# Performance work log

Hardware: AMD Instinct MI355X
Metric: run time of the kernel (lower is better)

Reference implementation:

```python
import jax, jax.numpy as jnp
import numpy as np

B, S, H, NH, F = 4, 1024, 1024, 16, 4096
HD = H // NH
PAD = 128  # last PAD positions are padding


def layer_norm(x, g, b, eps=1e-5):
    mu = jnp.mean(x, axis=-1, keepdims=True)
    var = jnp.mean(jnp.square(x - mu), axis=-1, keepdims=True)
    return (x - mu) * jax.lax.rsqrt(var + eps) * g + b


def setup_inputs() -> dict:
    key = jax.random.key(0)
    ks = jax.random.split(key, 10)
    sc = 0.02
    x = jax.random.normal(ks[0], (B, S, H), dtype=jnp.float32)
    attn_bias = jax.random.normal(ks[1], (B, S, S), dtype=jnp.float32)
    key_padding_mask = jnp.broadcast_to(jnp.arange(S) >= (S - PAD), (B, S))
    return {
        "x": x,
        "attn_bias": attn_bias,
        "key_padding_mask": key_padding_mask,
        "qkv_w": jax.random.normal(ks[2], (H, 3 * H), dtype=jnp.float32) * sc,
        "qkv_b": jnp.zeros((3 * H,), jnp.float32),
        "proj_w": jax.random.normal(ks[3], (H, H), dtype=jnp.float32) * sc,
        "proj_b": jnp.zeros((H,), jnp.float32),
        "ln1_g": jnp.ones((H,), jnp.float32),
        "ln1_b": jnp.zeros((H,), jnp.float32),
        "ln2_g": jnp.ones((H,), jnp.float32),
        "ln2_b": jnp.zeros((H,), jnp.float32),
        "ffn_w1": jax.random.normal(ks[4], (H, F), dtype=jnp.float32) * sc,
        "ffn_b1": jnp.zeros((F,), jnp.float32),
        "ffn_w2": jax.random.normal(ks[5], (F, H), dtype=jnp.float32) * sc,
        "ffn_b2": jnp.zeros((H,), jnp.float32),
    }


def reference(x, attn_bias, key_padding_mask, qkv_w, qkv_b, proj_w, proj_b,
              ln1_g, ln1_b, ln2_g, ln2_b, ffn_w1, ffn_b1, ffn_w2, ffn_b2):
    scale = HD ** -0.5
    qkv = (x @ qkv_w + qkv_b).reshape(B, S, 3, NH, HD)
    q, k, v = (qkv[:, :, i].transpose(0, 2, 1, 3) for i in range(3))  # [B,NH,S,HD]
    scores = jnp.einsum('bhqd,bhkd->bhqk', q, k) * scale
    scores = scores + attn_bias[:, None, :, :]
    scores = jnp.where(key_padding_mask[:, None, None, :], -jnp.inf, scores)
    attn = jax.nn.softmax(scores, axis=-1)
    out = jnp.einsum('bhqk,bhkd->bhqd', attn, v)
    out = out.transpose(0, 2, 1, 3).reshape(B, S, H)
    out = out @ proj_w + proj_b
    x = layer_norm(x + out, ln1_g, ln1_b)
    h = jax.nn.gelu(x @ ffn_w1 + ffn_b1, approximate=False)
    x = layer_norm(x + (h @ ffn_w2 + ffn_b2), ln2_g, ln2_b)
    x = jnp.where(key_padding_mask[:, :, None], 0.0, x)
    return x
```

## Files before the change

kernel.cpp:

```cpp
#include <hip/hip_runtime.h>
#include <cstdint>
#include <cstddef>

#define SEQ    1024
#define HDIM   1024
#define NHEAD  16
#define HEADD  64
#define FDIM   4096
#define BROWS  4096
#define SACT   896

typedef unsigned short u16;
typedef __bf16 bf16x8 __attribute__((ext_vector_type(8)));
typedef float  f32x4  __attribute__((ext_vector_type(4)));

__device__ __forceinline__ float bf2f(u16 u) {
    union { float f; unsigned v; } x; x.v = ((unsigned)u) << 16; return x.f;
}
__device__ __forceinline__ u16 f2bf(float f) {
    union { float f; unsigned v; } x; x.f = f;
    unsigned r = x.v + 0x7FFFu + ((x.v >> 16) & 1u);
    return (u16)(r >> 16);
}

__device__ __forceinline__ f32x4 mfma16(bf16x8 a, bf16x8 b, f32x4 c) {
    return __builtin_amdgcn_mfma_f32_16x16x32_bf16(a, b, c, 0, 0, 0);
}

__device__ __forceinline__ void gload16(const void* g, void* lds) {
    __builtin_amdgcn_global_load_lds(
        (__attribute__((address_space(1))) void*)g,
        (__attribute__((address_space(3))) void*)lds,
        16, 0, 0);
}

__global__ void cvt_bf16_kernel(const float* __restrict__ in, u16* __restrict__ out) {
    int i = blockIdx.x * 256 + threadIdx.x;
    float4 v = ((const float4*)in)[i];
    ushort4 o;
    o.x = f2bf(v.x); o.y = f2bf(v.y); o.z = f2bf(v.z); o.w = f2bf(v.w);
    ((ushort4*)out)[i] = o;
}

__global__ void wcvt_kernel(const float* __restrict__ W, u16* __restrict__ WT, int K, int N) {
    __shared__ float t[32][33];
    int n0 = blockIdx.x * 32, k0 = blockIdx.y * 32;
    int tx = threadIdx.x, ty = threadIdx.y;
    #pragma unroll
    for (int i = 0; i < 32; i += 8)
        t[ty + i][tx] = W[(size_t)(k0 + ty + i) * N + n0 + tx];
    __syncthreads();
    #pragma unroll
    for (int i = 0; i < 32; i += 8)
        WT[(size_t)(n0 + ty + i) * K + k0 + tx] = f2bf(t[tx][ty + i]);
}

__global__ void transpose_v_kernel(const u16* __restrict__ qkv, u16* __restrict__ vt) {
    __shared__ u16 t[64][65];
    int bh = blockIdx.y, b = bh >> 4, h = bh & 15;
    int s0 = blockIdx.x << 6;
    int tid = threadIdx.x;
    #pragma unroll
    for (int it = 0; it < 16; ++it) {
        int idx = tid + (it << 8);
        int r = idx >> 6, c = idx & 63;
        t[r][c] = qkv[(size_t)(b * SEQ + s0 + r) * 3072 + 2048 + h * 64 + c];
    }
    __syncthreads();
    #pragma unroll
    for (int it = 0; it < 16; ++it) {
        int idx = tid + (it << 8);
        int hd = idx >> 6, s = idx & 63;
        vt[((size_t)bh * 64 + hd) * SEQ + s0 + s] = t[s][hd];
    }
}

template<int EPI, int SPLITK>
__global__ __launch_bounds__(256, 2)
void gemm_kernel(const u16* __restrict__ A, const u16* __restrict__ Bt,
                 const float* __restrict__ bias, const float* __restrict__ res,
                 void* __restrict__ out, float* __restrict__ out1,
                 int M, int N, int K)
{
    __shared__ char smem[32768];
    char* sA = smem;
    char* sB = smem + 16384;
    const int tid  = threadIdx.x;
    const int wv   = tid >> 6, ln = tid & 63;
    const int lcol = ln & 15, quad = ln >> 4;
    const int wy   = wv >> 1, wx = wv & 1;
    const int mbase = blockIdx.x << 7, nbase = blockIdx.y << 7;

    int kstart = 0, kend = K;
    if (SPLITK) { int kh = K >> 1; kstart = blockIdx.z * kh; kend = kstart + kh; }

    f32x4 acc[4][4];
    #pragma unroll
    for (int i = 0; i < 4; ++i)
        #pragma unroll
        for (int j = 0; j < 4; ++j)
            acc[i][j] = (f32x4){0.f, 0.f, 0.f, 0.f};

    for (int k0 = kstart; k0 < kend; k0 += 64) {
        __syncthreads();
        #pragma unroll
        for (int c = 0; c < 4; ++c) {
            int base = (c * 4 + wv) << 10;
            int flat = base + (ln << 4);
            int row  = flat >> 7;
            int g    = ((flat >> 4) & 7) ^ (row & 7);
            gload16(A  + (size_t)(mbase + row) * K + k0 + g * 8, sA + base);
            gload16(Bt + (size_t)(nbase + row) * K + k0 + g * 8, sB + base);
        }
        __syncthreads();
        #pragma unroll
        for (int ks = 0; ks < 2; ++ks) {
            bf16x8 af[4], bfr[4];
            #pragma unroll
            for (int t = 0; t < 4; ++t) {
                int row = (wy << 6) + (t << 4) + lcol;
                int ca  = ((ks << 2) + quad) ^ (row & 7);
                af[t] = *(const bf16x8*)(sA + row * 128 + ca * 16);
                int nrow = (wx << 6) + (t << 4) + lcol;
                int cb  = ((ks << 2) + quad) ^ (nrow & 7);
                bfr[t] = *(const bf16x8*)(sB + nrow * 128 + cb * 16);
            }
            #pragma unroll
            for (int i = 0; i < 4; ++i)
                #pragma unroll
                for (int j = 0; j < 4; ++j)
                    acc[i][j] = mfma16(af[i], bfr[j], acc[i][j]);
        }
    }

    const bool partial = SPLITK && (blockIdx.z == 1);
    #pragma unroll
    for (int i = 0; i < 4; ++i) {
        #pragma unroll
        for (int r = 0; r < 4; ++r) {
            int grow = mbase + (wy << 6) + (i << 4) + (quad << 2) + r;
            #pragma unroll
            for (int j = 0; j < 4; ++j) {
                int gcol = nbase + (wx << 6) + (j << 4) + lcol;
                float v = acc[i][j][r];
                if (partial) {
                    out1[(size_t)grow * N + gcol] = v;
                    continue;
                }
                v += bias[gcol];
                if (EPI == 1 || EPI == 3) v += res[(size_t)grow * N + gcol];
                if (EPI == 2) v = 0.5f * v * (1.0f + erff(v * 0.70710678f));
                if (EPI == 0 || EPI == 2)
                    ((u16*)out)[(size_t)grow * N + gcol] = f2bf(v);
                else
                    ((float*)out)[(size_t)grow * N + gcol] = v;
            }
        }
    }
}

__global__ __launch_bounds__(256, 4)
void attn_kernel(const u16* __restrict__ qkv, const u16* __restrict__ vt,
                 const float* __restrict__ bias, u16* __restrict__ out)
{
    __shared__ char sK[2][8192];
    __shared__ char sV[2][8192];
    __shared__ char pbuf[4][2048];
    const int tid  = threadIdx.x;
    const int wid  = tid >> 6, lane = tid & 63;
    const int lcol = lane & 15, quad = lane >> 4;
    const int bh = blockIdx.y, b = bh >> 4, h = bh & 15;
    const int q0 = (blockIdx.x << 6) + (wid << 4);
    char* pb = pbuf[wid];
    const float LOG2E = 1.44269504088896f;

    const u16* qrow = qkv + (size_t)(b * SEQ + q0 + lcol) * 3072 + h * 64;
    bf16x8 qf[2];
    #pragma unroll
    for (int half = 0; half < 2; ++half) {
        union { bf16x8 v; u16 u[8]; } a;
        a.v = *(const bf16x8*)(qrow + half * 32 + quad * 8);
        #pragma unroll
        for (int j = 0; j < 8; ++j) a.u[j] = f2bf(bf2f(a.u[j]) * (0.125f * LOG2E));
        qf[half] = a.v;
    }

    f32x4 o[4];
    #pragma unroll
    for (int nt = 0; nt < 4; ++nt) o[nt] = (f32x4){0.f, 0.f, 0.f, 0.f};
    float lsum[4] = {0.f, 0.f, 0.f, 0.f};

    const u16* khead = qkv + (size_t)b * SEQ * 3072 + 1024 + h * 64;
    const u16* vhead = vt + (size_t)bh * 64 * SEQ;
    const float* bbase = bias + ((size_t)b * SEQ + q0 + quad * 4) * SEQ + lcol;

    auto stage = [&](int kb, int bufi) {
        #pragma unroll
        for (int i = 0; i < 2; ++i) {
            int ck  = i * 256 + tid;
            int row = ck >> 3, c = ck & 7;
            int g   = c ^ (row & 7);
            gload16(khead + (size_t)(kb + row) * 3072 + g * 8, sK[bufi] + ck * 16);
            gload16(vhead + (size_t)row * SEQ + kb + g * 8,    sV[bufi] + ck * 16);
        }
    };

    stage(0, 0);
    float bpre[4][4];
    #pragma unroll
    for (int i = 0; i < 4; ++i)
        #pragma unroll
        for (int j = 0; j < 4; ++j)
            bpre[i][j] = bbase[(size_t)i * SEQ + 16 * j] * LOG2E;
    __syncthreads();

    const int NT = SACT / 64;
    for (int t = 0; t < NT; ++t) {
        const int cur = t & 1, nxt = cur ^ 1;
        const int kb  = t << 6;

        if (t + 1 < NT) stage(kb + 64, nxt);

        f32x4 sc[4];
        #pragma unroll
        for (int j = 0; j < 4; ++j) sc[j] = (f32x4){0.f, 0.f, 0.f, 0.f};
        #pragma unroll
        for (int ks = 0; ks < 2; ++ks)
            #pragma unroll
            for (int j = 0; j < 4; ++j) {
                int n = j * 16 + lcol;
                int c = ((ks << 2) + quad) ^ (n & 7);
                bf16x8 kf = *(const bf16x8*)(sK[cur] + n * 128 + c * 16);
                sc[j] = mfma16(qf[ks], kf, sc[j]);
            }

        #pragma unroll
        for (int j = 0; j < 4; ++j)
            #pragma unroll
            for (int i = 0; i < 4; ++i)
                sc[j][i] += bpre[i][j];

        if (t + 1 < NT) {
            #pragma unroll
            for (int i = 0; i < 4; ++i)
                #pragma unroll
                for (int j = 0; j < 4; ++j)
                    bpre[i][j] = bbase[(size_t)i * SEQ + kb + 64 + 16 * j] * LOG2E;
        }

        #pragma unroll
        for (int i = 0; i < 4; ++i) {
            int row = quad * 4 + i;
            #pragma unroll
            for (int j = 0; j < 4; ++j) {
                float p = __builtin_amdgcn_exp2f(sc[j][i]);
                lsum[i] += p;
                union { float f; unsigned v; } u; u.f = p;
                int col = lcol + 16 * j;
                int cch = (col >> 3) ^ (row & 7);
                *(u16*)(pb + row * 128 + cch * 16 + (col & 7) * 2)
                    = (u16)((u.v + 0x8000u) >> 16);
            }
        }

        #pragma unroll
        for (int ks = 0; ks < 2; ++ks) {
            int cp = ((ks << 2) + quad) ^ (lcol & 7);
            bf16x8 pa = *(const bf16x8*)(pb + lcol * 128 + cp * 16);
            #pragma unroll
            for (int nt = 0; nt < 4; ++nt) {
                int d = nt * 16 + lcol;
                int c = ((ks << 2) + quad) ^ (d & 7);
                bf16x8 vf = *(const bf16x8*)(sV[cur] + d * 128 + c * 16);
                o[nt] = mfma16(pa, vf, o[nt]);
            }
        }

        __syncthreads();
    }

    #pragma unroll
    for (int off = 1; off < 16; off <<= 1)
        #pragma unroll
        for (int i = 0; i < 4; ++i)
            lsum[i] += __shfl_xor(lsum[i], off);

    float inv[4];
    #pragma unroll
    for (int i = 0; i < 4; ++i) inv[i] = 1.0f / lsum[i];
    #pragma unroll
    for (int nt = 0; nt < 4; ++nt)
        #pragma unroll
        for (int i = 0; i < 4; ++i)
            out[(size_t)(b * SEQ + q0 + quad * 4 + i) * HDIM + h * 64 + nt * 16 + lcol]
                = f2bf(o[nt][i] * inv[i]);
}

template<int MODE, int ADD2>
__global__ void ln_kernel(const float* __restrict__ y, const float* __restrict__ y2,
                          const float* __restrict__ g, const float* __restrict__ bt,
                          float* __restrict__ of32, u16* __restrict__ obf)
{
    int row = blockIdx.x;
    int tid = threadIdx.x;
    if (MODE == 1) {
        int s = row & (SEQ - 1);
        if (s >= SACT) {
            float4 z = {0.f, 0.f, 0.f, 0.f};
            ((float4*)(of32 + (size_t)row * HDIM))[tid] = z;
            return;
        }
    }
    float4 v = ((const float4*)(y + (size_t)row * HDIM))[tid];
    if (ADD2) {
        float4 w = ((const float4*)(y2 + (size_t)row * HDIM))[tid];
        v.x += w.x; v.y += w.y; v.z += w.z; v.w += w.w;
    }
    float s1 = v.x + v.y + v.z + v.w;
    float s2 = v.x * v.x + v.y * v.y + v.z * v.z + v.w * v.w;
    #pragma unroll
    for (int off = 32; off >= 1; off >>= 1) {
        s1 += __shfl_xor(s1, off);
        s2 += __shfl_xor(s2, off);
    }
    __shared__ float rs[8];
    int wv = tid >> 6, ln = tid & 63;
    if (ln == 0) { rs[wv] = s1; rs[4 + wv] = s2; }
    __syncthreads();
    s1 = rs[0] + rs[1] + rs[2] + rs[3];
    s2 = rs[4] + rs[5] + rs[6] + rs[7];
    float mean = s1 * (1.0f / 1024.0f);
    float var  = s2 * (1.0f / 1024.0f) - mean * mean;
    float rstd = rsqrtf(var + 1e-5f);
    float4 gg = ((const float4*)g)[tid];
    float4 bb = ((const float4*)bt)[tid];
    float4 o;
    o.x = (v.x - mean) * rstd * gg.x + bb.x;
    o.y = (v.y - mean) * rstd * gg.y + bb.y;
    o.z = (v.z - mean) * rstd * gg.z + bb.z;
    o.w = (v.w - mean) * rstd * gg.w + bb.w;
    ((float4*)(of32 + (size_t)row * HDIM))[tid] = o;
    if (MODE == 0) {
        ushort4 ob;
        ob.x = f2bf(o.x); ob.y = f2bf(o.y); ob.z = f2bf(o.z); ob.w = f2bf(o.w);
        ((ushort4*)(obf + (size_t)row * HDIM))[tid] = ob;
    }
}

extern "C" void kernel_launch(void* const* d_in, const int* in_sizes, int n_in,
                              void* d_out, int out_size, void* d_ws, size_t ws_size,
                              hipStream_t stream)
{
    const float* x      = (const float*)d_in[0];
    const float* abias  = (const float*)d_in[1];
    const float* qkv_w  = (const float*)d_in[3];
    const float* qkv_b  = (const float*)d_in[4];
    const float* proj_w = (const float*)d_in[5];
    const float* proj_b = (const float*)d_in[6];
    const float* ln1_g  = (const float*)d_in[7];
    const float* ln1_b  = (const float*)d_in[8];
    const float* ln2_g  = (const float*)d_in[9];
    const float* ln2_b  = (const float*)d_in[10];
    const float* w1     = (const float*)d_in[11];
    const float* b1     = (const float*)d_in[12];
    const float* w2     = (const float*)d_in[13];
    const float* b2     = (const float*)d_in[14];
    float* out = (float*)d_out;

    char* ws = (char*)d_ws;
    const size_t MB = 1024 * 1024;
    u16*  xb     = (u16*)(ws + 0);
    u16*  aout   = xb;
    u16*  qkvb   = (u16*)(ws + 8 * MB);
    u16*  vtb    = (u16*)(ws + 32 * MB);
    u16*  hb     = (u16*)(ws + 8 * MB);
    u16*  wqkvT  = (u16*)(ws + 40 * MB);
    u16*  wprojT = (u16*)(ws + 46 * MB);
    u16*  w1T    = (u16*)(ws + 48 * MB);
    u16*  w2T    = (u16*)(ws + 56 * MB);
    u16*  x1b    = (u16*)(ws + 64 * MB);
    float* ybuf  = (float*)(ws + 72 * MB);
    float* x1f   = (float*)(ws + 88 * MB);
    float* pproj = (float*)(ws + 8 * MB);
    float* pffn2 = (float*)(ws + 40 * MB);
    (void)in_sizes; (void)n_in; (void)out_size; (void)ws_size;

    dim3 tb32(32, 8);
    cvt_bf16_kernel<<<4096, 256, 0, stream>>>(x, xb);
    wcvt_kernel<<<dim3(3072 / 32, 1024 / 32), tb32, 0, stream>>>(qkv_w, wqkvT, 1024, 3072);
    wcvt_kernel<<<dim3(1024 / 32, 1024 / 32), tb32, 0, stream>>>(proj_w, wprojT, 1024, 1024);
    wcvt_kernel<<<dim3(4096 / 32, 1024 / 32), tb32, 0, stream>>>(w1, w1T, 1024, 4096);
    wcvt_kernel<<<dim3(1024 / 32, 4096 / 32), tb32, 0, stream>>>(w2, w2T, 4096, 1024);
    gemm_kernel<0, 0><<<dim3(32, 24), 256, 0, stream>>>(xb, wqkvT, qkv_b, nullptr, qkvb, nullptr, BROWS, 3072, 1024);
    transpose_v_kernel<<<dim3(16, 64), 256, 0, stream>>>(qkvb, vtb);
    attn_kernel<<<dim3(16, 64), 256, 0, stream>>>(qkvb, vtb, abias, aout);
    gemm_kernel<1, 1><<<dim3(32, 8, 2), 256, 0, stream>>>(aout, wprojT, proj_b, x, ybuf, pproj, BROWS, 1024, 1024);
    ln_kernel<0, 1><<<4096, 256, 0, stream>>>(ybuf, pproj, ln1_g, ln1_b, x1f, x1b);
    gemm_kernel<2, 0><<<dim3(32, 32), 256, 0, stream>>>(x1b, w1T, b1, nullptr, hb, nullptr, BROWS, 4096, 1024);
    gemm_kernel<3, 1><<<dim3(32, 8, 2), 256, 0, stream>>>(hb, w2T, b2, x1f, ybuf, pffn2, BROWS, 1024, 4096);
    ln_kernel<1, 1><<<4096, 256, 0, stream>>>(ybuf, pffn2, ln2_g, ln2_b, out, nullptr);
}
```

Before: 366.4 us.

## Use 4-way split-K with bf16 partials reduced in fused layernorm, merge prep kernels

Raises split-K for the projection and FFN2 GEMMs from 2 to 4. Each split writes bf16 partials, and the layernorm kernel sums them together with the residual and bias. The five conversion and transpose launches are merged into one prep kernel. The aim is to fill more CUs on the N=1024 GEMMs and cut launch overhead. In exchange, partial sums are rounded to bf16, which loses some precision.

```diff
diff --git a/kernel.cpp b/kernel.cpp
--- a/kernel.cpp
+++ b/kernel.cpp
@@ -14,6 +14,8 @@
 typedef __bf16 bf16x8 __attribute__((ext_vector_type(8)));
 typedef float  f32x4  __attribute__((ext_vector_type(4)));
 
+struct P4 { u16* p0; u16* p1; u16* p2; u16* p3; };
+
 __device__ __forceinline__ float bf2f(u16 u) {
     union { float f; unsigned v; } x; x.v = ((unsigned)u) << 16; return x.f;
 }
@@ -34,18 +36,29 @@
         16, 0, 0);
 }
 
-__global__ void cvt_bf16_kernel(const float* __restrict__ in, u16* __restrict__ out) {
-    int i = blockIdx.x * 256 + threadIdx.x;
-    float4 v = ((const float4*)in)[i];
-    ushort4 o;
-    o.x = f2bf(v.x); o.y = f2bf(v.y); o.z = f2bf(v.z); o.w = f2bf(v.w);
-    ((ushort4*)out)[i] = o;
-}
-
-__global__ void wcvt_kernel(const float* __restrict__ W, u16* __restrict__ WT, int K, int N) {
+__global__ void prep_kernel(const float* __restrict__ x, u16* __restrict__ xb,
+                            const float* __restrict__ qkvw, u16* __restrict__ wqkvT,
+                            const float* __restrict__ projw, u16* __restrict__ wprojT,
+                            const float* __restrict__ w1, u16* __restrict__ w1T,
+                            const float* __restrict__ w2, u16* __restrict__ w2T)
+{
+    int bid = blockIdx.x, tid = threadIdx.x;
+    if (bid < 4096) {
+        int i = bid * 256 + tid;
+        float4 v = ((const float4*)x)[i];
+        ushort4 o;
+        o.x = f2bf(v.x); o.y = f2bf(v.y); o.z = f2bf(v.z); o.w = f2bf(v.w);
+        ((ushort4*)xb)[i] = o;
+        return;
+    }
+    const float* W; u16* WT; int K, N, bxx, byy;
+    if (bid < 7168)       { int l = bid - 4096;  W = qkvw;  WT = wqkvT;  K = 1024; N = 3072; bxx = l % 96;  byy = l / 96; }
+    else if (bid < 8192)  { int l = bid - 7168;  W = projw; WT = wprojT; K = 1024; N = 1024; bxx = l % 32;  byy = l / 32; }
+    else if (bid < 12288) { int l = bid - 8192;  W = w1;    WT = w1T;    K = 1024; N = 4096; bxx = l % 128; byy = l / 128; }
+    else                  { int l = bid - 12288; W = w2;    WT = w2T;    K = 4096; N = 1024; bxx = l % 32;  byy = l / 32; }
     __shared__ float t[32][33];
-    int n0 = blockIdx.x * 32, k0 = blockIdx.y * 32;
-    int tx = threadIdx.x, ty = threadIdx.y;
+    int tx = tid & 31, ty = tid >> 5;
+    int n0 = bxx * 32, k0 = byy * 32;
     #pragma unroll
     for (int i = 0; i < 32; i += 8)
         t[ty + i][tx] = W[(size_t)(k0 + ty + i) * N + n0 + tx];
@@ -78,9 +91,8 @@
 template<int EPI, int SPLITK>
 __global__ __launch_bounds__(256, 2)
 void gemm_kernel(const u16* __restrict__ A, const u16* __restrict__ Bt,
-                 const float* __restrict__ bias, const float* __restrict__ res,
-                 void* __restrict__ out, float* __restrict__ out1,
-                 int M, int N, int K)
+                 const float* __restrict__ bias, void* __restrict__ out,
+                 P4 parts, int M, int N, int K)
 {
     __shared__ char smem[32768];
     char* sA = smem;
@@ -92,7 +104,7 @@
     const int mbase = blockIdx.x << 7, nbase = blockIdx.y << 7;
 
     int kstart = 0, kend = K;
-    if (SPLITK) { int kh = K >> 1; kstart = blockIdx.z * kh; kend = kstart + kh; }
+    if (SPLITK > 1) { int kq = K / SPLITK; kstart = blockIdx.z * kq; kend = kstart + kq; }
 
     f32x4 acc[4][4];
     #pragma unroll
@@ -133,7 +145,10 @@
         }
     }
 
-    const bool partial = SPLITK && (blockIdx.z == 1);
+    u16* op = nullptr;
+    if (SPLITK > 1)
+        op = (blockIdx.z == 0) ? parts.p0 : (blockIdx.z == 1) ? parts.p1
+           : (blockIdx.z == 2) ? parts.p2 : parts.p3;
     #pragma unroll
     for (int i = 0; i < 4; ++i) {
         #pragma unroll
@@ -143,17 +158,13 @@
             for (int j = 0; j < 4; ++j) {
                 int gcol = nbase + (wx << 6) + (j << 4) + lcol;
                 float v = acc[i][j][r];
-                if (partial) {
-                    out1[(size_t)grow * N + gcol] = v;
-                    continue;
+                if (SPLITK > 1) {
+                    op[(size_t)grow * N + gcol] = f2bf(v);
+                } else {
+                    v += bias[gcol];
+                    if (EPI == 2) v = 0.5f * v * (1.0f + erff(v * 0.70710678f));
+                    ((u16*)out)[(size_t)grow * N + gcol] = f2bf(v);
                 }
-                v += bias[gcol];
-                if (EPI == 1 || EPI == 3) v += res[(size_t)grow * N + gcol];
-                if (EPI == 2) v = 0.5f * v * (1.0f + erff(v * 0.70710678f));
-                if (EPI == 0 || EPI == 2)
-                    ((u16*)out)[(size_t)grow * N + gcol] = f2bf(v);
-                else
-                    ((float*)out)[(size_t)grow * N + gcol] = v;
             }
         }
     }
@@ -296,10 +307,12 @@
                 = f2bf(o[nt][i] * inv[i]);
 }
 
-template<int MODE, int ADD2>
-__global__ void ln_kernel(const float* __restrict__ y, const float* __restrict__ y2,
-                          const float* __restrict__ g, const float* __restrict__ bt,
-                          float* __restrict__ of32, u16* __restrict__ obf)
+template<int MODE>
+__global__ void ln_fused_kernel(const u16* __restrict__ p0, const u16* __restrict__ p1,
+                                const u16* __restrict__ p2, const u16* __restrict__ p3,
+                                const float* __restrict__ res, const float* __restrict__ cb,
+                                const float* __restrict__ g, const float* __restrict__ bt,
+                                float* __restrict__ of32, u16* __restrict__ obf)
 {
     int row = blockIdx.x;
     int tid = threadIdx.x;
@@ -311,11 +324,19 @@
             return;
         }
     }
-    float4 v = ((const float4*)(y + (size_t)row * HDIM))[tid];
-    if (ADD2) {
-        float4 w = ((const float4*)(y2 + (size_t)row * HDIM))[tid];
-        v.x += w.x; v.y += w.y; v.z += w.z; v.w += w.w;
-    }
+    size_t rb = (size_t)row * HDIM;
+    ushort4 a0 = ((const ushort4*)(p0 + rb))[tid];
+    ushort4 a1 = ((const ushort4*)(p1 + rb))[tid];
+    ushort4 a2 = ((const ushort4*)(p2 + rb))[tid];
+    ushort4 a3 = ((const ushort4*)(p3 + rb))[tid];
+    float4 r = ((const float4*)(res + rb))[tid];
+    float4 c = ((const float4*)cb)[tid];
+    float4 v;
+    v.x = bf2f(a0.x) + bf2f(a1.x) + bf2f(a2.x) + bf2f(a3.x) + r.x + c.x;
+    v.y = bf2f(a0.y) + bf2f(a1.y) + bf2f(a2.y) + bf2f(a3.y) + r.y + c.y;
+    v.z = bf2f(a0.z) + bf2f(a1.z) + bf2f(a2.z) + bf2f(a3.z) + r.z + c.z;
+    v.w = bf2f(a0.w) + bf2f(a1.w) + bf2f(a2.w) + bf2f(a3.w) + r.w + c.w;
+
     float s1 = v.x + v.y + v.z + v.w;
     float s2 = v.x * v.x + v.y * v.y + v.z * v.z + v.w * v.w;
     #pragma unroll
@@ -339,11 +360,11 @@
     o.y = (v.y - mean) * rstd * gg.y + bb.y;
     o.z = (v.z - mean) * rstd * gg.z + bb.z;
     o.w = (v.w - mean) * rstd * gg.w + bb.w;
-    ((float4*)(of32 + (size_t)row * HDIM))[tid] = o;
+    ((float4*)(of32 + rb))[tid] = o;
     if (MODE == 0) {
         ushort4 ob;
         ob.x = f2bf(o.x); ob.y = f2bf(o.y); ob.z = f2bf(o.z); ob.w = f2bf(o.w);
-        ((ushort4*)(obf + (size_t)row * HDIM))[tid] = ob;
+        ((ushort4*)(obf + rb))[tid] = ob;
     }
 }
 
@@ -370,7 +391,7 @@
     char* ws = (char*)d_ws;
     const size_t MB = 1024 * 1024;
     u16*  xb     = (u16*)(ws + 0);
-    u16*  aout   = xb;
+    u16*  aout   = (u16*)(ws + 0);
     u16*  qkvb   = (u16*)(ws + 8 * MB);
     u16*  vtb    = (u16*)(ws + 32 * MB);
     u16*  hb     = (u16*)(ws + 8 * MB);
@@ -379,24 +400,24 @@
     u16*  w1T    = (u16*)(ws + 48 * MB);
     u16*  w2T    = (u16*)(ws + 56 * MB);
     u16*  x1b    = (u16*)(ws + 64 * MB);
-    float* ybuf  = (float*)(ws + 72 * MB);
-    float* x1f   = (float*)(ws + 88 * MB);
-    float* pproj = (float*)(ws + 8 * MB);
-    float* pffn2 = (float*)(ws + 40 * MB);
+    float* x1f   = (float*)(ws + 72 * MB);
+    P4 projP = { (u16*)(ws + 8 * MB),  (u16*)(ws + 16 * MB),
+                 (u16*)(ws + 24 * MB), (u16*)(ws + 32 * MB) };
+    P4 ffn2P = { (u16*)(ws + 48 * MB), (u16*)(ws + 64 * MB),
+                 (u16*)(ws + 0),       (u16*)(ws + 40 * MB) };
+    P4 nullP = { nullptr, nullptr, nullptr, nullptr };
     (void)in_sizes; (void)n_in; (void)out_size; (void)ws_size;
 
-    dim3 tb32(32, 8);
-    cvt_bf16_kernel<<<4096, 256, 0, stream>>>(x, xb);
-    wcvt_kernel<<<dim3(3072 / 32, 1024 / 32), tb32, 0, stream>>>(qkv_w, wqkvT, 1024, 3072);
-    wcvt_kernel<<<dim3(1024 / 32, 1024 / 32), tb32, 0, stream>>>(proj_w, wprojT, 1024, 1024);
-    wcvt_kernel<<<dim3(4096 / 32, 1024 / 32), tb32, 0, stream>>>(w1, w1T, 1024, 4096);
-    wcvt_kernel<<<dim3(1024 / 32, 4096 / 32), tb32, 0, stream>>>(w2, w2T, 4096, 1024);
-    gemm_kernel<0, 0><<<dim3(32, 24), 256, 0, stream>>>(xb, wqkvT, qkv_b, nullptr, qkvb, nullptr, BROWS, 3072, 1024);
+    prep_kernel<<<16384, 256, 0, stream>>>(x, xb, qkv_w, wqkvT, proj_w, wprojT,
+                                           w1, w1T, w2, w2T);
+    gemm_kernel<0, 1><<<dim3(32, 24), 256, 0, stream>>>(xb, wqkvT, qkv_b, qkvb, nullP, BROWS, 3072, 1024);
     transpose_v_kernel<<<dim3(16, 64), 256, 0, stream>>>(qkvb, vtb);
     attn_kernel<<<dim3(16, 64), 256, 0, stream>>>(qkvb, vtb, abias, aout);
-    gemm_kernel<1, 1><<<dim3(32, 8, 2), 256, 0, stream>>>(aout, wprojT, proj_b, x, ybuf, pproj, BROWS, 1024, 1024);
-    ln_kernel<0, 1><<<4096, 256, 0, stream>>>(ybuf, pproj, ln1_g, ln1_b, x1f, x1b);
-    gemm_kernel<2, 0><<<dim3(32, 32), 256, 0, stream>>>(x1b, w1T, b1, nullptr, hb, nullptr, BROWS, 4096, 1024);
-    gemm_kernel<3, 1><<<dim3(32, 8, 2), 256, 0, stream>>>(hb, w2T, b2, x1f, ybuf, pffn2, BROWS, 1024, 4096);
-    ln_kernel<1, 1><<<4096, 256, 0, stream>>>(ybuf, pffn2, ln2_g, ln2_b, out, nullptr);
-}
+    gemm_kernel<0, 4><<<dim3(32, 8, 4), 256, 0, stream>>>(aout, wprojT, nullptr, nullptr, projP, BROWS, 1024, 1024);
+    ln_fused_kernel<0><<<4096, 256, 0, stream>>>(projP.p0, projP.p1, projP.p2, projP.p3,
+                                                 x, proj_b, ln1_g, ln1_b, x1f, x1b);
+    gemm_kernel<2, 1><<<dim3(32, 32), 256, 0, stream>>>(x1b, w1T, b1, hb, nullP, BROWS, 4096, 1024);
+    gemm_kernel<0, 4><<<dim3(32, 8, 4), 256, 0, stream>>>(hb, w2T, nullptr, nullptr, ffn2P, BROWS, 1024, 4096);
+    ln_fused_kernel<1><<<4096, 256, 0, stream>>>(ffn2P.p0, ffn2P.p1, ffn2P.p2, ffn2P.p3,
+                                                 x1f, b2, ln2_g, ln2_b, out, nullptr);
+}
```

Result: faster. 351.6 us (-4.0%).
